# Performance work log

Measured on AMD Instinct MI355X. Metric: run time of the kernel, lower is better.

The kernel has to match this reference:

```python
import jax, jax.numpy as jnp
import numpy as np

L = 16          # num_slices
RMIN, RMAX = 0.4, 0.9
B_, C_, H_, W_, N_ = 2, 4, 64, 64, 64   # n = 64 scan steps, last dim of x = N_*L


def setup_inputs() -> dict:
    key = jax.random.key(0)
    k = jax.random.split(key, 8)
    u1 = jax.random.uniform(k[0], (L,), dtype=jnp.float32)
    u2 = jax.random.uniform(k[1], (L,), dtype=jnp.float32)
    theta = 2.0 * np.pi * u2
    nu_log = jnp.log(-0.5 * jnp.log(u1 * (RMAX ** 2 - RMIN ** 2) + RMIN ** 2))
    # torch.complex(exp(-exp(nu_log)), theta): real part = modulus-like term, imag = theta
    Lambda_re = jnp.exp(-jnp.exp(nu_log))
    Lambda_im = theta
    B_re = jax.random.normal(k[2], (L, L), dtype=jnp.float32)
    B_im = jax.random.normal(k[3], (L, L), dtype=jnp.float32)
    C_re = jax.random.normal(k[4], (L, L), dtype=jnp.float32)
    C_im = jax.random.normal(k[5], (L, L), dtype=jnp.float32)
    D = jax.random.normal(k[6], (L, L), dtype=jnp.float32)
    x = jax.random.normal(k[7], (B_, C_, H_, W_, N_ * L), dtype=jnp.float32)
    return {"x": x, "Lambda_re": Lambda_re, "Lambda_im": Lambda_im,
            "B_re": B_re, "B_im": B_im, "C_re": C_re, "C_im": C_im, "D": D}


def reference(x, Lambda_re, Lambda_im, B_re, B_im, C_re, C_im, D):
    l = Lambda_re.shape[0]
    b, c, h, w, nl = x.shape
    n = nl // l
    img = x.reshape(b, c, h, w, n, l)                       # 'b c h w (n l) -> b c h w n l'
    Lam = jax.lax.complex(Lambda_re, Lambda_im)             # (l,) complex64
    Bc = jax.lax.complex(B_re, B_im)                        # (l,l) complex64
    Cc = jax.lax.complex(C_re, C_im)
    out = img.astype(jnp.complex64)
    # Faithful Hillis-Steele loop with op(x, y) = Lambda*x + B @ y
    for d in range(1, int(np.log2(n)) + 1):
        step = 2 ** (d - 1)
        left = out[..., : n - step, :]
        right = out[..., step:, :]
        new = left * Lam + jnp.einsum('kl,bchwnl->bchwnk', Bc, right)
        out = jnp.concatenate([out[..., :step, :], new], axis=-2)
    y = jnp.real(jnp.einsum('kl,bchwnl->bchwnk', Cc, out)) \
        + jnp.einsum('kl,bchwnl->bchwnk', D, img)
    return y
```

## Files before the change

### kernel.cpp

```cpp
#include <hip/hip_runtime.h>


namespace {

typedef __attribute__((ext_vector_type(8))) short short8v;
typedef __attribute__((ext_vector_type(4))) float f32x4;

__device__ inline unsigned short f2bf_rne(float f) {
    unsigned u = __builtin_bit_cast(unsigned, f);
    u += 0x7fffu + ((u >> 16) & 1u);
    return (unsigned short)(u >> 16);
}

__device__ inline void gld_lds16(const unsigned short* g, unsigned short* l) {
    __builtin_amdgcn_global_load_lds(
        (const __attribute__((address_space(1))) unsigned int*)g,
        (__attribute__((address_space(3))) unsigned int*)l, 16, 0, 0);
}


__global__ __launch_bounds__(256) void prep_kernel(
    const float* __restrict__ X,
    const float* __restrict__ Lre, const float* __restrict__ Lim,
    const float* __restrict__ Bre, const float* __restrict__ Bim,
    const float* __restrict__ Cre, const float* __restrict__ Cim,
    const float* __restrict__ Dm,
    unsigned short* __restrict__ Wh, unsigned short* __restrict__ Xh)
{
    const int t = threadIdx.x;

    if (blockIdx.x < 4096) {
        const int i = blockIdx.x >> 6, j = blockIdx.x & 63;
        const int k = t >> 4, l = t & 15;

        const int n_g = i * 16 + k;
        const int k_g = j * 16 + l;
        const size_t widx = (((size_t)((n_g >> 8) * 32 + (k_g >> 5))) << 13)
                          + (((k_g >> 3) & 3) << 11) + ((n_g & 255) << 3) + (k_g & 7);

        if (j > i) { Wh[widx] = 0; return; }

        __shared__ float2 Bs[16][16];
        __shared__ float2 M[16][16];
        Bs[k][l] = make_float2(Bre[t], Bim[t]);
        M[k][l]  = make_float2(k == l ? 1.f : 0.f, 0.f);
        const int delta = i - j;
        __syncthreads();

        #pragma unroll
        for (int d = 0; d < 6; ++d) {
            const int s = 1 << d;
            if (delta & s) {
                const float lr = Lre[k], li = Lim[k];
                const float2 m0 = M[k][l];
                M[k][l] = make_float2(lr * m0.x - li * m0.y, lr * m0.y + li * m0.x);
                __syncthreads();
            } else if (j + (delta & (s - 1)) >= s) {
                float2 acc = make_float2(0.f, 0.f);
                #pragma unroll
                for (int m = 0; m < 16; ++m) {
                    const float2 b = Bs[k][m], v = M[m][l];
                    acc.x += b.x * v.x - b.y * v.y;
                    acc.y += b.x * v.y + b.y * v.x;
                }
                __syncthreads();
                M[k][l] = acc;
                __syncthreads();
            }
        }

        float w = 0.f;
        #pragma unroll
        for (int m = 0; m < 16; ++m) {
            const float2 v = M[m][l];
            w += Cre[k * 16 + m] * v.x - Cim[k * 16 + m] * v.y;
        }
        if (i == j) w += Dm[t];
        Wh[widx] = f2bf_rne(w);
    } else {
        const int sid = blockIdx.x - 4096;
        const int mt = sid >> 5;
        const int kc = sid & 31;
        const size_t tb = ((size_t)(mt * 32 + kc)) << 12;

        #pragma unroll
        for (int p = 0; p < 4; ++p) {
            const int f = p * 256 + t;
            const int row = f >> 3, c4 = f & 7;
            const float4 v = *reinterpret_cast<const float4*>(
                X + (size_t)(mt * 128 + row) * 1024 + kc * 32 + c4 * 4);
            ushort4 hv;
            hv.x = f2bf_rne(v.x);
            hv.y = f2bf_rne(v.y);
            hv.z = f2bf_rne(v.z);
            hv.w = f2bf_rne(v.w);
            const size_t o = tb + ((size_t)(c4 >> 1) << 10) + (row << 3) + ((c4 & 1) << 2);
            *reinterpret_cast<ushort4*>(Xh + o) = hv;
        }
    }
}

__global__ __launch_bounds__(256, 2) void gemm_cnt_kernel(
    const unsigned short* __restrict__ Xh,
    const unsigned short* __restrict__ Wh,
    float* __restrict__ Y, int mtiles)
{
    __shared__ alignas(16) unsigned short sA[3][4096];
    __shared__ alignas(16) unsigned short sB[3][8192];

    const int bid = blockIdx.x;
    const int sb = 3 - bid / mtiles;
    const int mt = bid % mtiles;
    const int t = threadIdx.x;
    const int wid = t >> 6, lane = t & 63;
    const int wr = wid >> 1, wc = wid & 1;
    const int l15 = lane & 15, lg = lane >> 4;
    const int nt = (sb + 1) * 8;

    f32x4 acc[4][8] = {};

    int afo[4], bfo[8];
    #pragma unroll
    for (int mm = 0; mm < 4; ++mm)
        afo[mm] = (lg << 10) + ((wr * 64 + mm * 16 + l15) << 3);
    #pragma unroll
    for (int nn = 0; nn < 8; ++nn)
        bfo[nn] = (lg << 11) + ((wc * 128 + nn * 16 + l15) << 3);

    auto stageT = [&](int b3, int tk) {
        unsigned short* bA = sA[b3];
        unsigned short* bB = sB[b3];
        const unsigned short* xa = Xh + (((size_t)(mt * 32 + tk)) << 12);
        const unsigned short* wb = Wh + (((size_t)(sb * 32 + tk)) << 13);
        gld_lds16(xa + t * 8,        bA + t * 8);
        gld_lds16(xa + 2048 + t * 8, bA + 2048 + t * 8);
        gld_lds16(wb + t * 8,        bB + t * 8);
        gld_lds16(wb + 2048 + t * 8, bB + 2048 + t * 8);
        gld_lds16(wb + 4096 + t * 8, bB + 4096 + t * 8);
        gld_lds16(wb + 6144 + t * 8, bB + 6144 + t * 8);
    };

    stageT(0, 0);
    stageT(1, 1);
    asm volatile("s_waitcnt vmcnt(6)" ::: "memory");
    __builtin_amdgcn_sched_barrier(0);
    __builtin_amdgcn_s_barrier();
    __builtin_amdgcn_sched_barrier(0);

    int c = 0, c2 = 2;
    for (int tk = 0; tk < nt; ++tk) {
        if (tk + 2 < nt) stageT(c2, tk + 2);

        short8v ah[4], bh[8];
        #pragma unroll
        for (int mm = 0; mm < 4; ++mm)
            ah[mm] = *reinterpret_cast<const short8v*>(sA[c] + afo[mm]);
        #pragma unroll
        for (int nn = 0; nn < 8; ++nn)
            bh[nn] = *reinterpret_cast<const short8v*>(sB[c] + bfo[nn]);

        __builtin_amdgcn_s_setprio(1);
        #pragma unroll
        for (int mm = 0; mm < 4; ++mm)
            #pragma unroll
            for (int nn = 0; nn < 8; ++nn)
                acc[mm][nn] = __builtin_amdgcn_mfma_f32_16x16x32_bf16(
                    ah[mm], bh[nn], acc[mm][nn], 0, 0, 0);
        __builtin_amdgcn_s_setprio(0);

        if (tk + 1 < nt) {
            if (tk + 2 < nt) {
                asm volatile("s_waitcnt vmcnt(6)" ::: "memory");
            } else {
                asm volatile("s_waitcnt vmcnt(0)" ::: "memory");
            }
            __builtin_amdgcn_sched_barrier(0);
            __builtin_amdgcn_s_barrier();
            __builtin_amdgcn_sched_barrier(0);
        }
        c = (c == 2) ? 0 : c + 1;
        c2 = (c2 == 2) ? 0 : c2 + 1;
    }

    #pragma unroll
    for (int mm = 0; mm < 4; ++mm) {
        const int grow = mt * 128 + wr * 64 + mm * 16 + lg * 4;
        #pragma unroll
        for (int nn = 0; nn < 8; ++nn) {
            const int gcol = sb * 256 + wc * 128 + nn * 16 + l15;
            #pragma unroll
            for (int q = 0; q < 4; ++q)
                Y[(size_t)(grow + q) * 1024 + gcol] = acc[mm][nn][q];
        }
    }
}

}

extern "C" void kernel_launch(void* const* d_in, const int* in_sizes, int n_in,
                              void* d_out, int out_size, void* d_ws, size_t ws_size,
                              hipStream_t stream) {
    const float* x   = (const float*)d_in[0];
    const float* Lre = (const float*)d_in[1];
    const float* Lim = (const float*)d_in[2];
    const float* Bre = (const float*)d_in[3];
    const float* Bim = (const float*)d_in[4];
    const float* Cre = (const float*)d_in[5];
    const float* Cim = (const float*)d_in[6];
    const float* Dm  = (const float*)d_in[7];
    float* y = (float*)d_out;

    const int positions = in_sizes[0] / 1024;
    const int mtiles = positions / 128;

    unsigned short* Wh = (unsigned short*)d_ws;
    unsigned short* Xh = Wh + 1024 * 1024;

    prep_kernel<<<4096 + mtiles * 32, 256, 0, stream>>>(
        x, Lre, Lim, Bre, Bim, Cre, Cim, Dm, Wh, Xh);
    gemm_cnt_kernel<<<mtiles * 4, 256, 0, stream>>>(Xh, Wh, y, mtiles);
}
```

Baseline: 119.6 us.

## Keep X in row-major bf16 layout and gather A tiles in the GEMM loader

The fp32-to-bf16 conversion of X now writes a plain row-major copy with 16-byte coalesced stores, instead of scattering into a pre-tiled layout. The GEMM's A-tile staging gathers 16-byte row chunks directly from that layout, and the LDS fragment offsets change to match. This makes the conversion pass cheaper and simpler. In exchange, the GEMM's global loads become strided across rows and the LDS reads may hit bank conflicts. The conversion grid is hardcoded to 2048 blocks, which assumes the test input size.

```diff
diff --git a/kernel.cpp b/kernel.cpp
--- a/kernel.cpp
+++ b/kernel.cpp
@@ -29,75 +29,70 @@
 {
     const int t = threadIdx.x;
 
-    if (blockIdx.x < 4096) {
-        const int i = blockIdx.x >> 6, j = blockIdx.x & 63;
-        const int k = t >> 4, l = t & 15;
-
-        const int n_g = i * 16 + k;
-        const int k_g = j * 16 + l;
-        const size_t widx = (((size_t)((n_g >> 8) * 32 + (k_g >> 5))) << 13)
-                          + (((k_g >> 3) & 3) << 11) + ((n_g & 255) << 3) + (k_g & 7);
-
-        if (j > i) { Wh[widx] = 0; return; }
-
-        __shared__ float2 Bs[16][16];
-        __shared__ float2 M[16][16];
-        Bs[k][l] = make_float2(Bre[t], Bim[t]);
-        M[k][l]  = make_float2(k == l ? 1.f : 0.f, 0.f);
-        const int delta = i - j;
-        __syncthreads();
-
-        #pragma unroll
-        for (int d = 0; d < 6; ++d) {
-            const int s = 1 << d;
-            if (delta & s) {
-                const float lr = Lre[k], li = Lim[k];
-                const float2 m0 = M[k][l];
-                M[k][l] = make_float2(lr * m0.x - li * m0.y, lr * m0.y + li * m0.x);
-                __syncthreads();
-            } else if (j + (delta & (s - 1)) >= s) {
-                float2 acc = make_float2(0.f, 0.f);
-                #pragma unroll
-                for (int m = 0; m < 16; ++m) {
-                    const float2 b = Bs[k][m], v = M[m][l];
-                    acc.x += b.x * v.x - b.y * v.y;
-                    acc.y += b.x * v.y + b.y * v.x;
-                }
-                __syncthreads();
-                M[k][l] = acc;
-                __syncthreads();
+    if (blockIdx.x >= 4096) {
+        const int sid = blockIdx.x - 4096;
+        #pragma unroll
+        for (int p = 0; p < 8; ++p) {
+            const size_t c8 = ((size_t)p * 2048 * 256 + (size_t)sid * 256 + t) * 8;
+            const float4 a = *reinterpret_cast<const float4*>(X + c8);
+            const float4 b = *reinterpret_cast<const float4*>(X + c8 + 4);
+            short8v hv;
+            hv[0] = (short)f2bf_rne(a.x); hv[1] = (short)f2bf_rne(a.y);
+            hv[2] = (short)f2bf_rne(a.z); hv[3] = (short)f2bf_rne(a.w);
+            hv[4] = (short)f2bf_rne(b.x); hv[5] = (short)f2bf_rne(b.y);
+            hv[6] = (short)f2bf_rne(b.z); hv[7] = (short)f2bf_rne(b.w);
+            *reinterpret_cast<short8v*>(Xh + c8) = hv;
+        }
+        return;
+    }
+
+    const int i = blockIdx.x >> 6, j = blockIdx.x & 63;
+    const int k = t >> 4, l = t & 15;
+
+    const int n_g = i * 16 + k;
+    const int k_g = j * 16 + l;
+    const size_t widx = (((size_t)((n_g >> 8) * 32 + (k_g >> 5))) << 13)
+                      + (((k_g >> 3) & 3) << 11) + ((n_g & 255) << 3) + (k_g & 7);
+
+    if (j > i) { Wh[widx] = 0; return; }
+
+    __shared__ float2 Bs[16][16];
+    __shared__ float2 M[16][16];
+    Bs[k][l] = make_float2(Bre[t], Bim[t]);
+    M[k][l]  = make_float2(k == l ? 1.f : 0.f, 0.f);
+    const int delta = i - j;
+    __syncthreads();
+
+    #pragma unroll
+    for (int d = 0; d < 6; ++d) {
+        const int s = 1 << d;
+        if (delta & s) {
+            const float lr = Lre[k], li = Lim[k];
+            const float2 m0 = M[k][l];
+            M[k][l] = make_float2(lr * m0.x - li * m0.y, lr * m0.y + li * m0.x);
+            __syncthreads();
+        } else if (j + (delta & (s - 1)) >= s) {
+            float2 acc = make_float2(0.f, 0.f);
+            #pragma unroll
+            for (int m = 0; m < 16; ++m) {
+                const float2 b = Bs[k][m], v = M[m][l];
+                acc.x += b.x * v.x - b.y * v.y;
+                acc.y += b.x * v.y + b.y * v.x;
             }
-        }
-
-        float w = 0.f;
-        #pragma unroll
-        for (int m = 0; m < 16; ++m) {
-            const float2 v = M[m][l];
-            w += Cre[k * 16 + m] * v.x - Cim[k * 16 + m] * v.y;
-        }
-        if (i == j) w += Dm[t];
-        Wh[widx] = f2bf_rne(w);
-    } else {
-        const int sid = blockIdx.x - 4096;
-        const int mt = sid >> 5;
-        const int kc = sid & 31;
-        const size_t tb = ((size_t)(mt * 32 + kc)) << 12;
-
-        #pragma unroll
-        for (int p = 0; p < 4; ++p) {
-            const int f = p * 256 + t;
-            const int row = f >> 3, c4 = f & 7;
-            const float4 v = *reinterpret_cast<const float4*>(
-                X + (size_t)(mt * 128 + row) * 1024 + kc * 32 + c4 * 4);
-            ushort4 hv;
-            hv.x = f2bf_rne(v.x);
-            hv.y = f2bf_rne(v.y);
-            hv.z = f2bf_rne(v.z);
-            hv.w = f2bf_rne(v.w);
-            const size_t o = tb + ((size_t)(c4 >> 1) << 10) + (row << 3) + ((c4 & 1) << 2);
-            *reinterpret_cast<ushort4*>(Xh + o) = hv;
-        }
-    }
+            __syncthreads();
+            M[k][l] = acc;
+            __syncthreads();
+        }
+    }
+
+    float w = 0.f;
+    #pragma unroll
+    for (int m = 0; m < 16; ++m) {
+        const float2 v = M[m][l];
+        w += Cre[k * 16 + m] * v.x - Cim[k * 16 + m] * v.y;
+    }
+    if (i == j) w += Dm[t];
+    Wh[widx] = f2bf_rne(w);
 }
 
 __global__ __launch_bounds__(256, 2) void gemm_cnt_kernel(
@@ -122,18 +117,22 @@
     int afo[4], bfo[8];
     #pragma unroll
     for (int mm = 0; mm < 4; ++mm)
-        afo[mm] = (lg << 10) + ((wr * 64 + mm * 16 + l15) << 3);
+        afo[mm] = ((wr * 64 + mm * 16 + l15) << 5) + (lg << 3);
     #pragma unroll
     for (int nn = 0; nn < 8; ++nn)
         bfo[nn] = (lg << 11) + ((wc * 128 + nn * 16 + l15) << 3);
+
+    const int arow0 = t >> 2, akq = t & 3;
+    const size_t asrc0 = (size_t)arow0 * 1024 + akq * 8;
+    const size_t asrc1 = (size_t)(64 + arow0) * 1024 + akq * 8;
 
     auto stageT = [&](int b3, int tk) {
         unsigned short* bA = sA[b3];
         unsigned short* bB = sB[b3];
-        const unsigned short* xa = Xh + (((size_t)(mt * 32 + tk)) << 12);
+        const unsigned short* xa = Xh + ((size_t)mt << 17) + tk * 32;
         const unsigned short* wb = Wh + (((size_t)(sb * 32 + tk)) << 13);
-        gld_lds16(xa + t * 8,        bA + t * 8);
-        gld_lds16(xa + 2048 + t * 8, bA + 2048 + t * 8);
+        gld_lds16(xa + asrc0, bA + t * 8);
+        gld_lds16(xa + asrc1, bA + 2048 + t * 8);
         gld_lds16(wb + t * 8,        bB + t * 8);
         gld_lds16(wb + 2048 + t * 8, bB + 2048 + t * 8);
         gld_lds16(wb + 4096 + t * 8, bB + 4096 + t * 8);
@@ -216,7 +215,7 @@
     unsigned short* Wh = (unsigned short*)d_ws;
     unsigned short* Xh = Wh + 1024 * 1024;
 
-    prep_kernel<<<4096 + mtiles * 32, 256, 0, stream>>>(
+    prep_kernel<<<4096 + 2048, 256, 0, stream>>>(
         x, Lre, Lim, Bre, Bim, Cre, Cim, Dm, Wh, Xh);
     gemm_cnt_kernel<<<mtiles * 4, 256, 0, stream>>>(Xh, Wh, y, mtiles);
 }
```

After: 125.3 us. +4.7%, slower.
